# Performance work log

Hardware: AMD Instinct MI355X
Metric: run time of the kernel (lower is better)

The kernel has to match this reference:

```python
import jax, jax.numpy as jnp
import numpy as np

THETA = 10000.0

def _rope_cos_sin(seq_len, head_dim, dtype=jnp.float32):
    # matches precompute_freqs_cis: freqs over even indices of head_dim
    inv = 1.0 / (THETA ** (jnp.arange(0, head_dim, 2, dtype=jnp.float32) / head_dim))  # [hd/2]
    ang = jnp.arange(seq_len, dtype=jnp.float32)[:, None] * inv[None, :]               # [S, hd/2]
    return jnp.cos(ang).astype(dtype), jnp.sin(ang).astype(dtype)

def _apply_rope(x, cos, sin):
    # x: [b, h, s, d]; pairs are interleaved (d r) with r=2 -> complex (even=real, odd=imag)
    xe = x[..., 0::2]
    xo = x[..., 1::2]
    re = xe * cos - xo * sin
    im = xe * sin + xo * cos
    # interleave back: [..., d/2, 2] -> [..., d]
    return jnp.stack([re, im], axis=-1).reshape(x.shape)

def setup_inputs() -> dict:
    key = jax.random.key(0)
    ks = jax.random.split(key, 8)
    B, S, D = 2, 2048, 1024
    s = 0.02
    return {
        "query": jax.random.normal(ks[0], (B, S, D), jnp.float32),
        "key": jax.random.normal(ks[1], (B, S, D), jnp.float32),
        "value": jax.random.normal(ks[2], (B, S, D), jnp.float32),
        "q_w": jax.random.normal(ks[3], (D, D), jnp.float32) * s,
        "q_b": jnp.zeros((D,), jnp.float32),
        "k_w": jax.random.normal(ks[4], (D, D), jnp.float32) * s,
        "k_b": jnp.zeros((D,), jnp.float32),
        "v_w": jax.random.normal(ks[5], (D, D), jnp.float32) * s,
        "v_b": jnp.zeros((D,), jnp.float32),
        "o_w": jax.random.normal(ks[6], (D, D), jnp.float32) * s,
        "o_b": jnp.zeros((D,), jnp.float32),
    }

def reference(query, key, value, q_w, q_b, k_w, k_b, v_w, v_b, o_w, o_b):
    H = 16
    B, S, D = query.shape
    hd = D // H
    scaling = hd ** -0.5

    def split_heads(x):  # [b, s, (h d)] -> [b, h, s, d]
        return x.reshape(B, -1, H, hd).transpose(0, 2, 1, 3)

    q = split_heads(query @ q_w.T + q_b)
    k = split_heads(key @ k_w.T + k_b)
    v = split_heads(value @ v_w.T + v_b)

    cos, sin = _rope_cos_sin(S, hd)
    q = _apply_rope(q, cos, sin)
    k = _apply_rope(k, cos, sin)

    scores = jnp.einsum('bhqd,bhkd->bhqk', q, k) * scaling  # [B,H,S,S]
    attn = jax.nn.softmax(scores, axis=-1)
    out = jnp.einsum('bhqk,bhkd->bhqd', attn, v)            # [B,H,S,hd]
    out = out.transpose(0, 2, 1, 3).reshape(B, S, D)
    return out @ o_w.T + o_b
```

## Files before the change

### kernel.cpp

```cpp
#include <hip/hip_runtime.h>
#include <math.h>

#define B_  2
#define S_  2048
#define D_  1024
#define H_  16
#define HD_ 64
#define M_  (B_*S_)

typedef __attribute__((ext_vector_type(8))) short bf16x8;
typedef __attribute__((ext_vector_type(4))) float f32x4;
typedef unsigned short ushort_t;

#define MFMA32 __builtin_amdgcn_mfma_f32_16x16x32_bf16

__device__ inline unsigned short f2bf(float x) {
    unsigned u = __float_as_uint(x);
    unsigned r = (u + 0x7fff + ((u >> 16) & 1)) >> 16;
    return (unsigned short)r;
}
__device__ inline void gload16(const ushort_t* g, ushort_t* l) {
    __builtin_amdgcn_global_load_lds(
        (const __attribute__((address_space(1))) unsigned*)g,
        (__attribute__((address_space(3))) unsigned*)l, 16, 0, 0);
}

__global__ __launch_bounds__(256) void prep(
    const float* __restrict__ qa, const float* __restrict__ ka,
    const float* __restrict__ va,
    const float* __restrict__ qw, const float* __restrict__ kw,
    const float* __restrict__ vw, const float* __restrict__ ow,
    ushort_t* __restrict__ qab, ushort_t* __restrict__ kab,
    ushort_t* __restrict__ vab,
    ushort_t* __restrict__ qwb, ushort_t* __restrict__ kwb,
    ushort_t* __restrict__ vwb, ushort_t* __restrict__ owb,
    float* __restrict__ cost, float* __restrict__ sint)
{
    const int z = blockIdx.y;
    const int i = blockIdx.x * 256 + threadIdx.x;
    if (z == 7) {
        if (blockIdx.x >= (S_ * 32) / 256) return;
        int s = i >> 5, w = i & 31;
        double inv = pow(10000.0, -((double)(2 * w) / (double)HD_));
        double ang = (double)s * inv;
        cost[i] = (float)cos(ang);
        sint[i] = (float)sin(ang);
        return;
    }
    const float* in;
    ushort_t* dst;
    int n4;
    switch (z) {
        case 0: in = qa; dst = qab; n4 = (M_ * D_) / 4; break;
        case 1: in = ka; dst = kab; n4 = (M_ * D_) / 4; break;
        case 2: in = va; dst = vab; n4 = (M_ * D_) / 4; break;
        case 3: in = qw; dst = qwb; n4 = (D_ * D_) / 4; break;
        case 4: in = kw; dst = kwb; n4 = (D_ * D_) / 4; break;
        case 5: in = vw; dst = vwb; n4 = (D_ * D_) / 4; break;
        default: in = ow; dst = owb; n4 = (D_ * D_) / 4; break;
    }
    if (i >= n4) return;
    float4 v = ((const float4*)in)[i];
    unsigned short h0 = f2bf(v.x), h1 = f2bf(v.y), h2 = f2bf(v.z), h3 = f2bf(v.w);
    ((uint2*)dst)[i] = make_uint2((unsigned)h0 | ((unsigned)h1 << 16),
                                  (unsigned)h2 | ((unsigned)h3 << 16));
}

__global__ __launch_bounds__(256, 3) void fused_qkv(
    const ushort_t* __restrict__ A0, const ushort_t* __restrict__ A1,
    const ushort_t* __restrict__ A2,
    const ushort_t* __restrict__ W0, const ushort_t* __restrict__ W1,
    const ushort_t* __restrict__ W2,
    const float* __restrict__ b0, const float* __restrict__ b1,
    const float* __restrict__ b2,
    ushort_t* __restrict__ O0, ushort_t* __restrict__ O1,
    ushort_t* __restrict__ O2,
    const float* __restrict__ cost, const float* __restrict__ sint)
{
    __shared__ ushort_t Ab[12288];
    __shared__ ushort_t Wb[12288];

    const int tid  = threadIdx.x;
    const int wq   = tid >> 6;
    const int lane = tid & 63;
    const int l16  = lane & 15;
    const int quad = lane >> 4;

    const unsigned flat = blockIdx.x + (blockIdx.y << 3) + (blockIdx.z << 8);
    const unsigned xcd  = flat & 7;
    const unsigned slot = flat >> 3;
    const int z   = (int)(slot >> 5);
    const unsigned rr = slot & 31;
    const int bm  = (int)(xcd * 4 + (rr >> 3)) * 128;
    const int bn  = (int)(rr & 7) * 128;

    const ushort_t* A = z == 0 ? A0 : z == 1 ? A1 : A2;
    const ushort_t* W = z == 0 ? W0 : z == 1 ? W1 : W2;
    const float* bias = z == 0 ? b0 : z == 1 ? b1 : b2;

    const int m16 = tid & 15;
    const int akq = (tid >> 4) & 3;
    const int tw  = tid >> 6;

    const ushort_t* gA0 = A + (size_t)(bm + tw * 16 + m16) * D_ + akq * 8;
    const ushort_t* gA1 = gA0 + (size_t)64 * D_;
    const ushort_t* gW0 = W + (size_t)(bn + tw * 16 + m16) * D_ + akq * 8;
    const ushort_t* gW1 = gW0 + (size_t)64 * D_;

    const int wm = wq >> 1, wn = wq & 1;

    f32x4 acc[4][4];
#pragma unroll
    for (int mt = 0; mt < 4; ++mt)
#pragma unroll
        for (int nt = 0; nt < 4; ++nt)
            acc[mt][nt] = (f32x4){0.f, 0.f, 0.f, 0.f};

    gload16(gA0,      &Ab[tw * 512]);
    gload16(gA1,      &Ab[(tw + 4) * 512]);
    gload16(gW0,      &Wb[tw * 512]);
    gload16(gW1,      &Wb[(tw + 4) * 512]);
    gload16(gA0 + 32, &Ab[4096 + tw * 512]);
    gload16(gA1 + 32, &Ab[4096 + (tw + 4) * 512]);
    gload16(gW0 + 32, &Wb[4096 + tw * 512]);
    gload16(gW1 + 32, &Wb[4096 + (tw + 4) * 512]);

    int bcur = 0;
    for (int k = 0; k < 32; ++k) {
        if (k < 31) {
            asm volatile("s_waitcnt vmcnt(4)" ::: "memory");
        } else {
            asm volatile("s_waitcnt vmcnt(0)" ::: "memory");
        }
        __builtin_amdgcn_sched_barrier(0);
        __builtin_amdgcn_s_barrier();
        __builtin_amdgcn_sched_barrier(0);

        if (k < 30) {
            int bnx = bcur + 2; if (bnx >= 3) bnx -= 3;
            int ko = (k + 2) * 32;
            gload16(gA0 + ko, &Ab[bnx * 4096 + tw * 512]);
            gload16(gA1 + ko, &Ab[bnx * 4096 + (tw + 4) * 512]);
            gload16(gW0 + ko, &Wb[bnx * 4096 + tw * 512]);
            gload16(gW1 + ko, &Wb[bnx * 4096 + (tw + 4) * 512]);
        }

        const ushort_t* Abc = &Ab[bcur * 4096];
        const ushort_t* Wbc = &Wb[bcur * 4096];

        bf16x8 af[4], wf[4];
#pragma unroll
        for (int mt = 0; mt < 4; ++mt)
            af[mt] = *(const bf16x8*)&Abc[(wm * 4 + mt) * 512 + lane * 8];
#pragma unroll
        for (int nt = 0; nt < 4; ++nt)
            wf[nt] = *(const bf16x8*)&Wbc[(wn * 4 + nt) * 512 + lane * 8];
#pragma unroll
        for (int mt = 0; mt < 4; ++mt)
#pragma unroll
            for (int nt = 0; nt < 4; ++nt)
                acc[mt][nt] = MFMA32(af[mt], wf[nt], acc[mt][nt], 0, 0, 0);

        bcur += 1; if (bcur >= 3) bcur -= 3;
    }

    if (z == 0) {
        const float scale = 0.18033688011112042f;
#pragma unroll
        for (int mt = 0; mt < 4; ++mt) {
            int m = bm + wm * 64 + mt * 16 + quad * 4;
#pragma unroll
            for (int nt = 0; nt < 4; ++nt) {
                int n = bn + wn * 64 + nt * 16 + l16;
                float bb = bias[n];
                int h = n >> 6, d = n & 63, p = d >> 1;
#pragma unroll
                for (int r = 0; r < 4; ++r) {
                    int mm = m + r;
                    int s = mm & (S_ - 1), b = mm >> 11;
                    float x = acc[mt][nt][r] + bb;
                    float cs = cost[s * 32 + p], sn = sint[s * 32 + p];
                    float part = __shfl_xor(x, 1);
                    float y = (d & 1) ? (part * sn + x * cs)
                                      : (x * cs - part * sn);
                    O0[((size_t)(b * H_ + h) * S_ + s) * HD_ + d] = f2bf(y * scale);
                }
            }
        }
    } else if (z == 1) {
#pragma unroll
        for (int mt = 0; mt < 4; ++mt) {
            int m = bm + wm * 64 + mt * 16 + quad * 4;
#pragma unroll
            for (int nt = 0; nt < 4; ++nt) {
                int n = bn + wn * 64 + nt * 16 + l16;
                float bb = bias[n];
                int h = n >> 6, d = n & 63, p = d >> 1;
                int sub = ((d >> 5) & 1);
                int dq  = (d >> 3) & 3;
                int dj  = d & 7;
#pragma unroll
                for (int r = 0; r < 4; ++r) {
                    int mm = m + r;
                    int s = mm & (S_ - 1), b = mm >> 11;
                    float x = acc[mt][nt][r] + bb;
                    float cs = cost[s * 32 + p], sn = sint[s * 32 + p];
                    float part = __shfl_xor(x, 1);
                    float y = (d & 1) ? (part * sn + x * cs)
                                      : (x * cs - part * sn);
                    int kt  = s >> 5;
                    int st  = ((s >> 4) & 1) * 2 + sub;
                    size_t idx = ((size_t)(b * H_ + h) * 64 + kt) * 2048
                               + st * 512 + dq * 128 + (s & 15) * 8 + dj;
                    O1[idx] = f2bf(y);
                }
            }
        }
    } else {
#pragma unroll
        for (int mt = 0; mt < 4; ++mt) {
            int m = bm + wm * 64 + mt * 16 + quad * 4;
            int b = m >> 11, s0 = m & (S_ - 1);
            int vt = s0 >> 5;
            int kk = s0 & 31;
            int qd = (kk & 15) >> 2;
            int w0 = ((kk >> 4) & 1) * 4;
#pragma unroll
            for (int nt = 0; nt < 4; ++nt) {
                int n = bn + wn * 64 + nt * 16 + l16;
                float bb = bias[n];
                int h = n >> 6, d = n & 63;
                int mtv = d >> 4, dd = d & 15;
                unsigned short hh[4];
#pragma unroll
                for (int r = 0; r < 4; ++r)
                    hh[r] = f2bf(acc[mt][nt][r] + bb);
                size_t idx = ((size_t)(b * H_ + h) * 64 + vt) * 2048
                           + mtv * 512 + qd * 128 + dd * 8 + w0;
                *(uint2*)(O2 + idx) = make_uint2(
                    (unsigned)hh[0] | ((unsigned)hh[1] << 16),
                    (unsigned)hh[2] | ((unsigned)hh[3] << 16));
            }
        }
    }
}

__global__ __launch_bounds__(256, 2) void proj_o(
    const ushort_t* __restrict__ A, const ushort_t* __restrict__ W,
    const float* __restrict__ bias, float* __restrict__ outf)
{
    __shared__ ushort_t Ab[6144];
    __shared__ ushort_t Wb[12288];

    const int tid  = threadIdx.x;
    const int wq   = tid >> 6;
    const int lane = tid & 63;
    const int l16  = lane & 15;
    const int quad = lane >> 4;

    const unsigned flat = blockIdx.x + (blockIdx.y << 3);
    const unsigned xcd  = flat & 7;
    const unsigned slot = flat >> 3;
    const int bm = (int)(xcd * 8 + (slot >> 3)) * 64;
    const int bn = (int)(slot & 7) * 128;

    const int m16 = tid & 15;
    const int akq = (tid >> 4) & 3;
    const int tw  = tid >> 6;

    const ushort_t* gA  = A + (size_t)(bm + tw * 16 + m16) * D_ + akq * 8;
    const ushort_t* gW0 = W + (size_t)(bn + tw * 16 + m16) * D_ + akq * 8;
    const ushort_t* gW1 = gW0 + (size_t)64 * D_;

    const int wm = wq >> 1, wn = wq & 1;

    f32x4 acc[2][4];
#pragma unroll
    for (int mt = 0; mt < 2; ++mt)
#pragma unroll
        for (int nt = 0; nt < 4; ++nt)
            acc[mt][nt] = (f32x4){0.f, 0.f, 0.f, 0.f};

    gload16(gA,       &Ab[tw * 512]);
    gload16(gW0,      &Wb[tw * 512]);
    gload16(gW1,      &Wb[(tw + 4) * 512]);
    gload16(gA + 32,  &Ab[2048 + tw * 512]);
    gload16(gW0 + 32, &Wb[4096 + tw * 512]);
    gload16(gW1 + 32, &Wb[4096 + (tw + 4) * 512]);

    int bcur = 0;
    for (int k = 0; k < 32; ++k) {
        if (k < 31) {
            asm volatile("s_waitcnt vmcnt(3)" ::: "memory");
        } else {
            asm volatile("s_waitcnt vmcnt(0)" ::: "memory");
        }
        __builtin_amdgcn_sched_barrier(0);
        __builtin_amdgcn_s_barrier();
        __builtin_amdgcn_sched_barrier(0);

        if (k < 30) {
            int bnx = bcur + 2; if (bnx >= 3) bnx -= 3;
            int ko = (k + 2) * 32;
            gload16(gA  + ko, &Ab[bnx * 2048 + tw * 512]);
            gload16(gW0 + ko, &Wb[bnx * 4096 + tw * 512]);
            gload16(gW1 + ko, &Wb[bnx * 4096 + (tw + 4) * 512]);
        }

        const ushort_t* Abc = &Ab[bcur * 2048];
        const ushort_t* Wbc = &Wb[bcur * 4096];

        bf16x8 af[2], wf[4];
#pragma unroll
        for (int mt = 0; mt < 2; ++mt)
            af[mt] = *(const bf16x8*)&Abc[(wm * 2 + mt) * 512 + lane * 8];
#pragma unroll
        for (int nt = 0; nt < 4; ++nt)
            wf[nt] = *(const bf16x8*)&Wbc[(wn * 4 + nt) * 512 + lane * 8];
#pragma unroll
        for (int mt = 0; mt < 2; ++mt)
#pragma unroll
            for (int nt = 0; nt < 4; ++nt)
                acc[mt][nt] = MFMA32(af[mt], wf[nt], acc[mt][nt], 0, 0, 0);

        bcur += 1; if (bcur >= 3) bcur -= 3;
    }

#pragma unroll
    for (int mt = 0; mt < 2; ++mt) {
        int m = bm + wm * 32 + mt * 16 + quad * 4;
#pragma unroll
        for (int nt = 0; nt < 4; ++nt) {
            int n = bn + wn * 64 + nt * 16 + l16;
            float bb = bias[n];
#pragma unroll
            for (int r = 0; r < 4; ++r)
                outf[(size_t)(m + r) * D_ + n] = acc[mt][nt][r] + bb;
        }
    }
}

__global__ __launch_bounds__(256, 2) void attn_mfma(
    const ushort_t* __restrict__ Q, const ushort_t* __restrict__ Kf,
    const ushort_t* __restrict__ Vf, ushort_t* __restrict__ AO)
{
    __shared__ __align__(16) unsigned char SM[49152 + 512];
    float* MRG = (float*)SM;
    float* PSB = (float*)(SM + 49152);

    const int tid  = threadIdx.x;
    const int wq   = tid >> 6;
    const int lane = tid & 63;
    const int l16  = lane & 15;
    const int quad = lane >> 4;
    const int qg   = wq & 1;
    const int ks   = wq >> 1;

    const unsigned flat = blockIdx.x + (blockIdx.y << 4);
    const unsigned xcd  = flat & 7;
    const unsigned slot = flat >> 3;
    const int bh   = (int)(xcd * 4 + (slot >> 4));
    const int q0   = (int)(slot & 15) * 128 + qg * 64;

    bf16x8 qa[4][2];
#pragma unroll
    for (int nh = 0; nh < 4; ++nh)
#pragma unroll
        for (int c = 0; c < 2; ++c) {
            int row = q0 + nh * 16 + l16;
            qa[nh][c] = *(const bf16x8*)(Q + ((size_t)bh * S_ + row) * HD_
                                           + c * 32 + quad * 8);
        }
#pragma unroll
    for (int nh = 0; nh < 4; ++nh)
#pragma unroll
        for (int c = 0; c < 2; ++c)
            asm volatile("" : "+v"(qa[nh][c]));

    f32x4 oacc[4][4];
    f32x4 osum[4];
#pragma unroll
    for (int nh = 0; nh < 4; ++nh) {
        osum[nh] = (f32x4){0.f, 0.f, 0.f, 0.f};
#pragma unroll
        for (int mt = 0; mt < 4; ++mt)
            oacc[nh][mt] = (f32x4){0.f, 0.f, 0.f, 0.f};
    }

    const bf16x8 ones8 = {(short)0x3F80, (short)0x3F80, (short)0x3F80,
                          (short)0x3F80, (short)0x3F80, (short)0x3F80,
                          (short)0x3F80, (short)0x3F80};

    const ushort_t* Kbase = Kf + (size_t)bh * 64 * 2048;
    const ushort_t* Vbase = Vf + (size_t)bh * 64 * 2048;

#pragma unroll
    for (int t = 0; t < 2; ++t) {
        ushort_t* KB = (ushort_t*)(SM + t * 16384);
        ushort_t* VB = KB + 4096;
        const ushort_t* Kq = Kbase + (size_t)t * 4096;
        const ushort_t* Vq = Vbase + (size_t)t * 4096;
        gload16(Kq + tid * 8,        KB + tid * 8);
        gload16(Kq + 2048 + tid * 8, KB + 2048 + tid * 8);
        gload16(Vq + tid * 8,        VB + tid * 8);
        gload16(Vq + 2048 + tid * 8, VB + 2048 + tid * 8);
    }

    int cur = 0;
    for (int i = 0; i < 32; ++i) {
        if (i < 31) {
            asm volatile("s_waitcnt vmcnt(4)" ::: "memory");
        } else {
            asm volatile("s_waitcnt vmcnt(0)" ::: "memory");
        }
        __builtin_amdgcn_sched_barrier(0);
        __builtin_amdgcn_s_barrier();
        __builtin_amdgcn_sched_barrier(0);

        if (i < 30) {
            int nb = cur + 2; if (nb >= 3) nb -= 3;
            ushort_t* KB = (ushort_t*)(SM + nb * 16384);
            ushort_t* VB = KB + 4096;
            const ushort_t* Kq = Kbase + (size_t)(i + 2) * 4096;
            const ushort_t* Vq = Vbase + (size_t)(i + 2) * 4096;
            gload16(Kq + tid * 8,        KB + tid * 8);
            gload16(Kq + 2048 + tid * 8, KB + 2048 + tid * 8);
            gload16(Vq + tid * 8,        VB + tid * 8);
            gload16(Vq + 2048 + tid * 8, VB + 2048 + tid * 8);
        }

        const ushort_t* Kc = (const ushort_t*)(SM + cur * 16384) + ks * 2048;
        const ushort_t* Vc = (const ushort_t*)(SM + cur * 16384) + 4096 + ks * 2048;

        bf16x8 kf[2][2];
#pragma unroll
        for (int g = 0; g < 2; ++g)
#pragma unroll
            for (int c = 0; c < 2; ++c)
                kf[g][c] = *(const bf16x8*)&Kc[(g * 2 + c) * 512 + lane * 8];

        f32x4 s[4][2];
#pragma unroll
        for (int nh = 0; nh < 4; ++nh)
#pragma unroll
            for (int g = 0; g < 2; ++g)
                s[nh][g] = (f32x4){0.f, 0.f, 0.f, 0.f};
        __builtin_amdgcn_s_setprio(1);
#pragma unroll
        for (int c = 0; c < 2; ++c)
#pragma unroll
            for (int nh = 0; nh < 4; ++nh)
#pragma unroll
                for (int g = 0; g < 2; ++g)
                    s[nh][g] = MFMA32(kf[g][c], qa[nh][c], s[nh][g], 0, 0, 0);
        __builtin_amdgcn_s_setprio(0);

        bf16x8 pb8[4];
#pragma unroll
        for (int nh = 0; nh < 4; ++nh) {
            float p00 = __builtin_exp2f(s[nh][0][0]);
            float p01 = __builtin_exp2f(s[nh][0][1]);
            float p02 = __builtin_exp2f(s[nh][0][2]);
            float p03 = __builtin_exp2f(s[nh][0][3]);
            float p10 = __builtin_exp2f(s[nh][1][0]);
            float p11 = __builtin_exp2f(s[nh][1][1]);
            float p12 = __builtin_exp2f(s[nh][1][2]);
            float p13 = __builtin_exp2f(s[nh][1][3]);
            union { bf16x8 v; unsigned u[4]; } t;
            t.u[0] = __builtin_amdgcn_perm(__float_as_uint(p01),
                                           __float_as_uint(p00), 0x07060302);
            t.u[1] = __builtin_amdgcn_perm(__float_as_uint(p03),
                                           __float_as_uint(p02), 0x07060302);
            t.u[2] = __builtin_amdgcn_perm(__float_as_uint(p11),
                                           __float_as_uint(p10), 0x07060302);
            t.u[3] = __builtin_amdgcn_perm(__float_as_uint(p13),
                                           __float_as_uint(p12), 0x07060302);
            pb8[nh] = t.v;
        }

        __builtin_amdgcn_s_setprio(1);
#pragma unroll
        for (int mt = 0; mt < 4; ++mt) {
            bf16x8 vv = *(const bf16x8*)&Vc[mt * 512 + lane * 8];
#pragma unroll
            for (int nh = 0; nh < 4; ++nh)
                oacc[nh][mt] = MFMA32(vv, pb8[nh], oacc[nh][mt], 0, 0, 0);
        }
#pragma unroll
        for (int nh = 0; nh < 4; ++nh)
            osum[nh] = MFMA32(ones8, pb8[nh], osum[nh], 0, 0, 0);
        __builtin_amdgcn_s_setprio(0);

        cur += 1; if (cur >= 3) cur -= 3;
    }

    __syncthreads();

    if (ks == 1) {
#pragma unroll
        for (int nh = 0; nh < 4; ++nh) {
#pragma unroll
            for (int mt = 0; mt < 4; ++mt)
#pragma unroll
                for (int r = 0; r < 4; ++r)
                    MRG[(qg * 64 + nh * 16 + l16) * 65 + mt * 16 + quad * 4 + r]
                        = oacc[nh][mt][r];
            if (quad == 0)
                PSB[qg * 64 + nh * 16 + l16] = osum[nh][0];
        }
    }
    __syncthreads();
    if (ks == 0) {
        const int b = bh >> 4, h = bh & 15;
#pragma unroll
        for (int nh = 0; nh < 4; ++nh) {
            float pst = osum[nh][0] + PSB[qg * 64 + nh * 16 + l16];
            float inv = 1.0f / pst;
            int q = q0 + nh * 16 + l16;
#pragma unroll
            for (int mt = 0; mt < 4; ++mt) {
                unsigned short hh[4];
#pragma unroll
                for (int r = 0; r < 4; ++r) {
                    float x = oacc[nh][mt][r]
                        + MRG[(qg * 64 + nh * 16 + l16) * 65 + mt * 16 + quad * 4 + r];
                    hh[r] = f2bf(x * inv);
                }
                size_t base = ((size_t)b * S_ + q) * D_ + h * HD_
                            + mt * 16 + quad * 4;
                *(uint2*)(AO + base) = make_uint2(
                    (unsigned)hh[0] | ((unsigned)hh[1] << 16),
                    (unsigned)hh[2] | ((unsigned)hh[3] << 16));
            }
        }
    }
}

extern "C" void kernel_launch(void* const* d_in, const int* in_sizes, int n_in,
                              void* d_out, int out_size, void* d_ws, size_t ws_size,
                              hipStream_t stream) {
    const float* query = (const float*)d_in[0];
    const float* key   = (const float*)d_in[1];
    const float* value = (const float*)d_in[2];
    const float* q_w   = (const float*)d_in[3];
    const float* q_b   = (const float*)d_in[4];
    const float* k_w   = (const float*)d_in[5];
    const float* k_b   = (const float*)d_in[6];
    const float* v_w   = (const float*)d_in[7];
    const float* v_b   = (const float*)d_in[8];
    const float* o_w   = (const float*)d_in[9];
    const float* o_b   = (const float*)d_in[10];
    float* out = (float*)d_out;

    const size_t NT = (size_t)M_ * D_;
    const size_t WT = (size_t)D_ * D_;
    ushort_t* p = (ushort_t*)d_ws;
    ushort_t* qa_b = p; p += NT;
    ushort_t* ka_b = p; p += NT;
    ushort_t* va_b = p; p += NT;
    ushort_t* wqb  = p; p += WT;
    ushort_t* wkb  = p; p += WT;
    ushort_t* wvb  = p; p += WT;
    ushort_t* wob  = p; p += WT;
    ushort_t* Qb   = p; p += NT;
    ushort_t* Kfr  = p; p += NT;
    ushort_t* Vfr  = p; p += NT;
    ushort_t* AO   = p; p += NT;
    float* cost = (float*)p;
    float* sint = cost + (size_t)S_ * 32;

    dim3 gp((unsigned)(NT / 4 / 256), 8);
    prep<<<gp, 256, 0, stream>>>(query, key, value, q_w, k_w, v_w, o_w,
                                 qa_b, ka_b, va_b, wqb, wkb, wvb, wob,
                                 cost, sint);

    dim3 gq(D_ / 128, M_ / 128, 3);
    fused_qkv<<<gq, 256, 0, stream>>>(
        qa_b, ka_b, va_b, wqb, wkb, wvb,
        q_b, k_b, v_b, Qb, Kfr, Vfr, cost, sint);

    dim3 agrid(S_ / 128, B_ * H_);
    attn_mfma<<<agrid, 256, 0, stream>>>(Qb, Kfr, Vfr, AO);

    dim3 go(D_ / 128, M_ / 64);
    proj_o<<<go, 256, 0, stream>>>(AO, wob, o_b, out);
}
```

Before: 248.6 us.

## Restructure attention into 128-thread blocks without key-split merge

```diff
diff --git a/kernel.cpp b/kernel.cpp
--- a/kernel.cpp
+++ b/kernel.cpp
@@ -340,31 +340,27 @@
     }
 }
 
-__global__ __launch_bounds__(256, 2) void attn_mfma(
+__global__ __launch_bounds__(128, 3) void attn_mfma(
     const ushort_t* __restrict__ Q, const ushort_t* __restrict__ Kf,
     const ushort_t* __restrict__ Vf, ushort_t* __restrict__ AO)
 {
-    __shared__ __align__(16) unsigned char SM[49152 + 512];
-    float* MRG = (float*)SM;
-    float* PSB = (float*)(SM + 49152);
+    __shared__ __align__(16) ushort_t SMEM[3 * 4096];
 
     const int tid  = threadIdx.x;
     const int wq   = tid >> 6;
     const int lane = tid & 63;
     const int l16  = lane & 15;
     const int quad = lane >> 4;
-    const int qg   = wq & 1;
-    const int ks   = wq >> 1;
-
-    const unsigned flat = blockIdx.x + (blockIdx.y << 4);
+
+    const unsigned flat = blockIdx.x + (blockIdx.y << 5);
     const unsigned xcd  = flat & 7;
     const unsigned slot = flat >> 3;
-    const int bh   = (int)(xcd * 4 + (slot >> 4));
-    const int q0   = (int)(slot & 15) * 128 + qg * 64;
-
-    bf16x8 qa[4][2];
-#pragma unroll
-    for (int nh = 0; nh < 4; ++nh)
+    const int bh = (int)(xcd * 4 + (slot >> 5));
+    const int q0 = (int)(slot & 31) * 64 + wq * 32;
+
+    bf16x8 qa[2][2];
+#pragma unroll
+    for (int nh = 0; nh < 2; ++nh)
 #pragma unroll
         for (int c = 0; c < 2; ++c) {
             int row = q0 + nh * 16 + l16;
@@ -372,15 +368,15 @@
                                            + c * 32 + quad * 8);
         }
 #pragma unroll
-    for (int nh = 0; nh < 4; ++nh)
+    for (int nh = 0; nh < 2; ++nh)
 #pragma unroll
         for (int c = 0; c < 2; ++c)
             asm volatile("" : "+v"(qa[nh][c]));
 
-    f32x4 oacc[4][4];
-    f32x4 osum[4];
-#pragma unroll
-    for (int nh = 0; nh < 4; ++nh) {
+    f32x4 oacc[2][4];
+    f32x4 osum[2];
+#pragma unroll
+    for (int nh = 0; nh < 2; ++nh) {
         osum[nh] = (f32x4){0.f, 0.f, 0.f, 0.f};
 #pragma unroll
         for (int mt = 0; mt < 4; ++mt)
@@ -396,19 +392,18 @@
 
 #pragma unroll
     for (int t = 0; t < 2; ++t) {
-        ushort_t* KB = (ushort_t*)(SM + t * 16384);
-        ushort_t* VB = KB + 4096;
-        const ushort_t* Kq = Kbase + (size_t)t * 4096;
-        const ushort_t* Vq = Vbase + (size_t)t * 4096;
+        ushort_t* KB = &SMEM[t * 4096];
+        const ushort_t* Kq = Kbase + (size_t)t * 2048;
+        const ushort_t* Vq = Vbase + (size_t)t * 2048;
         gload16(Kq + tid * 8,        KB + tid * 8);
-        gload16(Kq + 2048 + tid * 8, KB + 2048 + tid * 8);
-        gload16(Vq + tid * 8,        VB + tid * 8);
-        gload16(Vq + 2048 + tid * 8, VB + 2048 + tid * 8);
+        gload16(Kq + 1024 + tid * 8, KB + 1024 + tid * 8);
+        gload16(Vq + tid * 8,        KB + 2048 + tid * 8);
+        gload16(Vq + 1024 + tid * 8, KB + 3072 + tid * 8);
     }
 
     int cur = 0;
-    for (int i = 0; i < 32; ++i) {
-        if (i < 31) {
+    for (int i = 0; i < 64; ++i) {
+        if (i < 63) {
             asm volatile("s_waitcnt vmcnt(4)" ::: "memory");
         } else {
             asm volatile("s_waitcnt vmcnt(0)" ::: "memory");
@@ -417,20 +412,19 @@
         __builtin_amdgcn_s_barrier();
         __builtin_amdgcn_sched_barrier(0);
 
-        if (i < 30) {
+        if (i < 62) {
             int nb = cur + 2; if (nb >= 3) nb -= 3;
-            ushort_t* KB = (ushort_t*)(SM + nb * 16384);
-            ushort_t* VB = KB + 4096;
-            const ushort_t* Kq = Kbase + (size_t)(i + 2) * 4096;
-            const ushort_t* Vq = Vbase + (size_t)(i + 2) * 4096;
+            ushort_t* KB = &SMEM[nb * 4096];
+            const ushort_t* Kq = Kbase + (size_t)(i + 2) * 2048;
+            const ushort_t* Vq = Vbase + (size_t)(i + 2) * 2048;
             gload16(Kq + tid * 8,        KB + tid * 8);
-            gload16(Kq + 2048 + tid * 8, KB + 2048 + tid * 8);
-            gload16(Vq + tid * 8,        VB + tid * 8);
-            gload16(Vq + 2048 + tid * 8, VB + 2048 + tid * 8);
-        }
-
-        const ushort_t* Kc = (const ushort_t*)(SM + cur * 16384) + ks * 2048;
-        const ushort_t* Vc = (const ushort_t*)(SM + cur * 16384) + 4096 + ks * 2048;
+            gload16(Kq + 1024 + tid * 8, KB + 1024 + tid * 8);
+            gload16(Vq + tid * 8,        KB + 2048 + tid * 8);
+            gload16(Vq + 1024 + tid * 8, KB + 3072 + tid * 8);
+        }
+
+        const ushort_t* Kc = &SMEM[cur * 4096];
+        const ushort_t* Vc = Kc + 2048;
 
         bf16x8 kf[2][2];
 #pragma unroll
@@ -439,9 +433,9 @@
             for (int c = 0; c < 2; ++c)
                 kf[g][c] = *(const bf16x8*)&Kc[(g * 2 + c) * 512 + lane * 8];
 
-        f32x4 s[4][2];
-#pragma unroll
-        for (int nh = 0; nh < 4; ++nh)
+        f32x4 s[2][2];
+#pragma unroll
+        for (int nh = 0; nh < 2; ++nh)
 #pragma unroll
             for (int g = 0; g < 2; ++g)
                 s[nh][g] = (f32x4){0.f, 0.f, 0.f, 0.f};
@@ -449,15 +443,15 @@
 #pragma unroll
         for (int c = 0; c < 2; ++c)
 #pragma unroll
-            for (int nh = 0; nh < 4; ++nh)
+            for (int nh = 0; nh < 2; ++nh)
 #pragma unroll
                 for (int g = 0; g < 2; ++g)
                     s[nh][g] = MFMA32(kf[g][c], qa[nh][c], s[nh][g], 0, 0, 0);
         __builtin_amdgcn_s_setprio(0);
 
-        bf16x8 pb8[4];
-#pragma unroll
-        for (int nh = 0; nh < 4; ++nh) {
+        bf16x8 pb8[2];
+#pragma unroll
+        for (int nh = 0; nh < 2; ++nh) {
             float p00 = __builtin_exp2f(s[nh][0][0]);
             float p01 = __builtin_exp2f(s[nh][0][1]);
             float p02 = __builtin_exp2f(s[nh][0][2]);
@@ -483,49 +477,29 @@
         for (int mt = 0; mt < 4; ++mt) {
             bf16x8 vv = *(const bf16x8*)&Vc[mt * 512 + lane * 8];
 #pragma unroll
-            for (int nh = 0; nh < 4; ++nh)
+            for (int nh = 0; nh < 2; ++nh)
                 oacc[nh][mt] = MFMA32(vv, pb8[nh], oacc[nh][mt], 0, 0, 0);
         }
 #pragma unroll
-        for (int nh = 0; nh < 4; ++nh)
+        for (int nh = 0; nh < 2; ++nh)
             osum[nh] = MFMA32(ones8, pb8[nh], osum[nh], 0, 0, 0);
         __builtin_amdgcn_s_setprio(0);
 
         cur += 1; if (cur >= 3) cur -= 3;
     }
 
-    __syncthreads();
-
-    if (ks == 1) {
-#pragma unroll
-        for (int nh = 0; nh < 4; ++nh) {
-#pragma unroll
-            for (int mt = 0; mt < 4; ++mt)
-#pragma unroll
-                for (int r = 0; r < 4; ++r)
-                    MRG[(qg * 64 + nh * 16 + l16) * 65 + mt * 16 + quad * 4 + r]
-                        = oacc[nh][mt][r];
-            if (quad == 0)
-                PSB[qg * 64 + nh * 16 + l16] = osum[nh][0];
-        }
-    }
-    __syncthreads();
-    if (ks == 0) {
+    {
         const int b = bh >> 4, h = bh & 15;
 #pragma unroll
-        for (int nh = 0; nh < 4; ++nh) {
-            float pst = osum[nh][0] + PSB[qg * 64 + nh * 16 + l16];
-            float inv = 1.0f / pst;
+        for (int nh = 0; nh < 2; ++nh) {
+            float inv = 1.0f / osum[nh][0];
             int q = q0 + nh * 16 + l16;
 #pragma unroll
             for (int mt = 0; mt < 4; ++mt) {
                 unsigned short hh[4];
 #pragma unroll
-                for (int r = 0; r < 4; ++r) {
-                    float x = oacc[nh][mt][r]
-                        + MRG[(qg * 64 + nh * 16 + l16) * 65 + mt * 16 + quad * 4 + r];
-                    hh[r] = f2bf(x * inv);
-                }
+                for (int r = 0; r < 4; ++r)
+                    hh[r] = f2bf(oacc[nh][mt][r] * inv);
                 size_t base = ((size_t)b * S_ + q) * D_ + h * HD_
                             + mt * 16 + quad * 4;
                 *(uint2*)(AO + base) = make_uint2(
@@ -579,8 +553,8 @@
         qa_b, ka_b, va_b, wqb, wkb, wvb,
         q_b, k_b, v_b, Qb, Kfr, Vfr, cost, sint);
 
-    dim3 agrid(S_ / 128, B_ * H_);
-    attn_mfma<<<agrid, 256, 0, stream>>>(Qb, Kfr, Vfr, AO);
+    dim3 agrid(S_ / 64, B_ * H_);
+    attn_mfma<<<agrid, 128, 0, stream>>>(Qb, Kfr, Vfr, AO);
 
     dim3 go(D_ / 128, M_ / 64);
     proj_o<<<go, 256, 0, stream>>>(AO, wob, o_b, out);
```

Measured after the change: 254.3 us. +2.3%, slower.

## Software-pipeline attention loop: overlap previous tile's PV MFMAs with exp2

Applied to the files above, without the earlier changes.

```diff
diff --git a/kernel.cpp b/kernel.cpp
--- a/kernel.cpp
+++ b/kernel.cpp
@@ -344,9 +344,9 @@
     const ushort_t* __restrict__ Q, const ushort_t* __restrict__ Kf,
     const ushort_t* __restrict__ Vf, ushort_t* __restrict__ AO)
 {
-    __shared__ __align__(16) unsigned char SM[49152 + 512];
+    __shared__ __align__(16) unsigned char SM[65536 + 512];
     float* MRG = (float*)SM;
-    float* PSB = (float*)(SM + 49152);
+    float* PSB = (float*)(SM + 65536);
 
     const int tid  = threadIdx.x;
     const int wq   = tid >> 6;
@@ -391,22 +391,25 @@
                           (short)0x3F80, (short)0x3F80, (short)0x3F80,
                           (short)0x3F80, (short)0x3F80};
 
+    bf16x8 pb8p[4];
+#pragma unroll
+    for (int nh = 0; nh < 4; ++nh)
+        pb8p[nh] = (bf16x8){0, 0, 0, 0, 0, 0, 0, 0};
+
     const ushort_t* Kbase = Kf + (size_t)bh * 64 * 2048;
     const ushort_t* Vbase = Vf + (size_t)bh * 64 * 2048;
 
 #pragma unroll
     for (int t = 0; t < 2; ++t) {
         ushort_t* KB = (ushort_t*)(SM + t * 16384);
-        ushort_t* VB = KB + 4096;
         const ushort_t* Kq = Kbase + (size_t)t * 4096;
         const ushort_t* Vq = Vbase + (size_t)t * 4096;
         gload16(Kq + tid * 8,        KB + tid * 8);
         gload16(Kq + 2048 + tid * 8, KB + 2048 + tid * 8);
-        gload16(Vq + tid * 8,        VB + tid * 8);
-        gload16(Vq + 2048 + tid * 8, VB + 2048 + tid * 8);
-    }
-
-    int cur = 0;
+        gload16(Vq + tid * 8,        KB + 4096 + tid * 8);
+        gload16(Vq + 2048 + tid * 8, KB + 4096 + 2048 + tid * 8);
+    }
+
     for (int i = 0; i < 32; ++i) {
         if (i < 31) {
             asm volatile("s_waitcnt vmcnt(4)" ::: "memory");
@@ -418,19 +421,19 @@
         __builtin_amdgcn_sched_barrier(0);
 
         if (i < 30) {
-            int nb = cur + 2; if (nb >= 3) nb -= 3;
+            const int nb = (i + 2) & 3;
             ushort_t* KB = (ushort_t*)(SM + nb * 16384);
-            ushort_t* VB = KB + 4096;
             const ushort_t* Kq = Kbase + (size_t)(i + 2) * 4096;
             const ushort_t* Vq = Vbase + (size_t)(i + 2) * 4096;
             gload16(Kq + tid * 8,        KB + tid * 8);
             gload16(Kq + 2048 + tid * 8, KB + 2048 + tid * 8);
-            gload16(Vq + tid * 8,        VB + tid * 8);
-            gload16(Vq + 2048 + tid * 8, VB + 2048 + tid * 8);
-        }
-
-        const ushort_t* Kc = (const ushort_t*)(SM + cur * 16384) + ks * 2048;
-        const ushort_t* Vc = (const ushort_t*)(SM + cur * 16384) + 4096 + ks * 2048;
+            gload16(Vq + tid * 8,        KB + 4096 + tid * 8);
+            gload16(Vq + 2048 + tid * 8, KB + 4096 + 2048 + tid * 8);
+        }
+
+        const ushort_t* Kc = (const ushort_t*)(SM + (i & 3) * 16384) + ks * 2048;
+        const int vb = i ? ((i - 1) & 3) : 0;
+        const ushort_t* Vc = (const ushort_t*)(SM + vb * 16384) + 4096 + ks * 2048;
 
         bf16x8 kf[2][2];
 #pragma unroll
@@ -438,6 +441,10 @@
 #pragma unroll
             for (int c = 0; c < 2; ++c)
                 kf[g][c] = *(const bf16x8*)&Kc[(g * 2 + c) * 512 + lane * 8];
+        bf16x8 vv[4];
+#pragma unroll
+        for (int mt = 0; mt < 4; ++mt)
+            vv[mt] = *(const bf16x8*)&Vc[mt * 512 + lane * 8];
 
         f32x4 s[4][2];
 #pragma unroll
@@ -453,9 +460,17 @@
 #pragma unroll
                 for (int g = 0; g < 2; ++g)
                     s[nh][g] = MFMA32(kf[g][c], qa[nh][c], s[nh][g], 0, 0, 0);
+
+#pragma unroll
+        for (int mt = 0; mt < 4; ++mt)
+#pragma unroll
+            for (int nh = 0; nh < 4; ++nh)
+                oacc[nh][mt] = MFMA32(vv[mt], pb8p[nh], oacc[nh][mt], 0, 0, 0);
+#pragma unroll
+        for (int nh = 0; nh < 4; ++nh)
+            osum[nh] = MFMA32(ones8, pb8p[nh], osum[nh], 0, 0, 0);
         __builtin_amdgcn_s_setprio(0);
 
-        bf16x8 pb8[4];
 #pragma unroll
         for (int nh = 0; nh < 4; ++nh) {
             float p00 = __builtin_exp2f(s[nh][0][0]);
@@ -475,23 +490,22 @@
                                            __float_as_uint(p10), 0x07060302);
             t.u[3] = __builtin_amdgcn_perm(__float_as_uint(p13),
                                            __float_as_uint(p12), 0x07060302);
-            pb8[nh] = t.v;
-        }
-
-        __builtin_amdgcn_s_setprio(1);
+            pb8p[nh] = t.v;
+        }
+    }
+
+    {
+        const ushort_t* Vc = (const ushort_t*)(SM + 3 * 16384) + 4096 + ks * 2048;
 #pragma unroll
         for (int mt = 0; mt < 4; ++mt) {
             bf16x8 vv = *(const bf16x8*)&Vc[mt * 512 + lane * 8];
 #pragma unroll
             for (int nh = 0; nh < 4; ++nh)
-                oacc[nh][mt] = MFMA32(vv, pb8[nh], oacc[nh][mt], 0, 0, 0);
+                oacc[nh][mt] = MFMA32(vv, pb8p[nh], oacc[nh][mt], 0, 0, 0);
         }
 #pragma unroll
         for (int nh = 0; nh < 4; ++nh)
-            osum[nh] = MFMA32(ones8, pb8[nh], osum[nh], 0, 0, 0);
-        __builtin_amdgcn_s_setprio(0);
-
-        cur += 1; if (cur >= 3) cur -= 3;
+            osum[nh] = MFMA32(ones8, pb8p[nh], osum[nh], 0, 0, 0);
     }
 
     __syncthreads();
```

New measurement: 248.3 us. No clear change (-0.1%).

## Load attention K/V fragments directly into registers with double-buffered prefetch

Applied to the files above, without the earlier changes.

```diff
diff --git a/kernel.cpp b/kernel.cpp
--- a/kernel.cpp
+++ b/kernel.cpp
@@ -340,13 +340,76 @@
     }
 }
 
+__device__ __forceinline__ void attn_body(
+    bf16x8 (&KR)[4], bf16x8 (&VR)[4], int i,
+    const bf16x8 (&qa)[4][2], f32x4 (&oacc)[4][4], f32x4 (&osum)[4],
+    const bf16x8& ones8, const ushort_t* kp, const ushort_t* vp)
+{
+    f32x4 s[4][2];
+#pragma unroll
+    for (int nh = 0; nh < 4; ++nh)
+#pragma unroll
+        for (int g = 0; g < 2; ++g)
+            s[nh][g] = (f32x4){0.f, 0.f, 0.f, 0.f};
+    __builtin_amdgcn_s_setprio(1);
+#pragma unroll
+    for (int c = 0; c < 2; ++c)
+#pragma unroll
+        for (int nh = 0; nh < 4; ++nh)
+#pragma unroll
+            for (int g = 0; g < 2; ++g)
+                s[nh][g] = MFMA32(KR[g * 2 + c], qa[nh][c], s[nh][g], 0, 0, 0);
+    __builtin_amdgcn_s_setprio(0);
+
+    bf16x8 pb8[4];
+#pragma unroll
+    for (int nh = 0; nh < 4; ++nh) {
+        float p00 = __builtin_exp2f(s[nh][0][0]);
+        float p01 = __builtin_exp2f(s[nh][0][1]);
+        float p02 = __builtin_exp2f(s[nh][0][2]);
+        float p03 = __builtin_exp2f(s[nh][0][3]);
+        float p10 = __builtin_exp2f(s[nh][1][0]);
+        float p11 = __builtin_exp2f(s[nh][1][1]);
+        float p12 = __builtin_exp2f(s[nh][1][2]);
+        float p13 = __builtin_exp2f(s[nh][1][3]);
+        union { bf16x8 v; unsigned u[4]; } t;
+        t.u[0] = __builtin_amdgcn_perm(__float_as_uint(p01),
+                                       __float_as_uint(p00), 0x07060302);
+        t.u[1] = __builtin_amdgcn_perm(__float_as_uint(p03),
+                                       __float_as_uint(p02), 0x07060302);
+        t.u[2] = __builtin_amdgcn_perm(__float_as_uint(p11),
+                                       __float_as_uint(p10), 0x07060302);
+        t.u[3] = __builtin_amdgcn_perm(__float_as_uint(p13),
+                                       __float_as_uint(p12), 0x07060302);
+        pb8[nh] = t.v;
+    }
+
+    __builtin_amdgcn_s_setprio(1);
+#pragma unroll
+    for (int mt = 0; mt < 4; ++mt)
+#pragma unroll
+        for (int nh = 0; nh < 4; ++nh)
+            oacc[nh][mt] = MFMA32(VR[mt], pb8[nh], oacc[nh][mt], 0, 0, 0);
+#pragma unroll
+    for (int nh = 0; nh < 4; ++nh)
+        osum[nh] = MFMA32(ones8, pb8[nh], osum[nh], 0, 0, 0);
+    __builtin_amdgcn_s_setprio(0);
+
+    if (i + 2 < 32) {
+#pragma unroll
+        for (int j = 0; j < 4; ++j) {
+            KR[j] = *(const bf16x8*)(kp + (size_t)(i + 2) * 4096 + j * 512);
+            VR[j] = *(const bf16x8*)(vp + (size_t)(i + 2) * 4096 + j * 512);
+        }
+    }
+}
+
 __global__ __launch_bounds__(256, 2) void attn_mfma(
     const ushort_t* __restrict__ Q, const ushort_t* __restrict__ Kf,
     const ushort_t* __restrict__ Vf, ushort_t* __restrict__ AO)
 {
-    __shared__ __align__(16) unsigned char SM[49152 + 512];
-    float* MRG = (float*)SM;
-    float* PSB = (float*)(SM + 49152);
+    __shared__ float MRG[128 * 65];
+    __shared__ float PSB[128];
 
     const int tid  = threadIdx.x;
     const int wq   = tid >> 6;
@@ -391,110 +454,22 @@
                           (short)0x3F80, (short)0x3F80, (short)0x3F80,
                           (short)0x3F80, (short)0x3F80};
 
-    const ushort_t* Kbase = Kf + (size_t)bh * 64 * 2048;
-    const ushort_t* Vbase = Vf + (size_t)bh * 64 * 2048;
-
-#pragma unroll
-    for (int t = 0; t < 2; ++t) {
-        ushort_t* KB = (ushort_t*)(SM + t * 16384);
-        ushort_t* VB = KB + 4096;
-        const ushort_t* Kq = Kbase + (size_t)t * 4096;
-        const ushort_t* Vq = Vbase + (size_t)t * 4096;
-        gload16(Kq + tid * 8,        KB + tid * 8);
-        gload16(Kq + 2048 + tid * 8, KB + 2048 + tid * 8);
-        gload16(Vq + tid * 8,        VB + tid * 8);
-        gload16(Vq + 2048 + tid * 8, VB + 2048 + tid * 8);
-    }
-
-    int cur = 0;
-    for (int i = 0; i < 32; ++i) {
-        if (i < 31) {
-            asm volatile("s_waitcnt vmcnt(4)" ::: "memory");
-        } else {
-            asm volatile("s_waitcnt vmcnt(0)" ::: "memory");
-        }
-        __builtin_amdgcn_sched_barrier(0);
-        __builtin_amdgcn_s_barrier();
-        __builtin_amdgcn_sched_barrier(0);
-
-        if (i < 30) {
-            int nb = cur + 2; if (nb >= 3) nb -= 3;
-            ushort_t* KB = (ushort_t*)(SM + nb * 16384);
-            ushort_t* VB = KB + 4096;
-            const ushort_t* Kq = Kbase + (size_t)(i + 2) * 4096;
-            const ushort_t* Vq = Vbase + (size_t)(i + 2) * 4096;
-            gload16(Kq + tid * 8,        KB + tid * 8);
-            gload16(Kq + 2048 + tid * 8, KB + 2048 + tid * 8);
-            gload16(Vq + tid * 8,        VB + tid * 8);
-            gload16(Vq + 2048 + tid * 8, VB + 2048 + tid * 8);
-        }
-
-        const ushort_t* Kc = (const ushort_t*)(SM + cur * 16384) + ks * 2048;
-        const ushort_t* Vc = (const ushort_t*)(SM + cur * 16384) + 4096 + ks * 2048;
-
-        bf16x8 kf[2][2];
-#pragma unroll
-        for (int g = 0; g < 2; ++g)
-#pragma unroll
-            for (int c = 0; c < 2; ++c)
-                kf[g][c] = *(const bf16x8*)&Kc[(g * 2 + c) * 512 + lane * 8];
-
-        f32x4 s[4][2];
-#pragma unroll
-        for (int nh = 0; nh < 4; ++nh)
-#pragma unroll
-            for (int g = 0; g < 2; ++g)
-                s[nh][g] = (f32x4){0.f, 0.f, 0.f, 0.f};
-        __builtin_amdgcn_s_setprio(1);
-#pragma unroll
-        for (int c = 0; c < 2; ++c)
-#pragma unroll
-            for (int nh = 0; nh < 4; ++nh)
-#pragma unroll
-                for (int g = 0; g < 2; ++g)
-                    s[nh][g] = MFMA32(kf[g][c], qa[nh][c], s[nh][g], 0, 0, 0);
-        __builtin_amdgcn_s_setprio(0);
-
-        bf16x8 pb8[4];
-#pragma unroll
-        for (int nh = 0; nh < 4; ++nh) {
-            float p00 = __builtin_exp2f(s[nh][0][0]);
-            float p01 = __builtin_exp2f(s[nh][0][1]);
-            float p02 = __builtin_exp2f(s[nh][0][2]);
-            float p03 = __builtin_exp2f(s[nh][0][3]);
-            float p10 = __builtin_exp2f(s[nh][1][0]);
-            float p11 = __builtin_exp2f(s[nh][1][1]);
-            float p12 = __builtin_exp2f(s[nh][1][2]);
-            float p13 = __builtin_exp2f(s[nh][1][3]);
-            union { bf16x8 v; unsigned u[4]; } t;
-            t.u[0] = __builtin_amdgcn_perm(__float_as_uint(p01),
-                                           __float_as_uint(p00), 0x07060302);
-            t.u[1] = __builtin_amdgcn_perm(__float_as_uint(p03),
-                                           __float_as_uint(p02), 0x07060302);
-            t.u[2] = __builtin_amdgcn_perm(__float_as_uint(p11),
-                                           __float_as_uint(p10), 0x07060302);
-            t.u[3] = __builtin_amdgcn_perm(__float_as_uint(p13),
-                                           __float_as_uint(p12), 0x07060302);
-            pb8[nh] = t.v;
-        }
-
-        __builtin_amdgcn_s_setprio(1);
-#pragma unroll
-        for (int mt = 0; mt < 4; ++mt) {
-            bf16x8 vv = *(const bf16x8*)&Vc[mt * 512 + lane * 8];
-#pragma unroll
-            for (int nh = 0; nh < 4; ++nh)
-                oacc[nh][mt] = MFMA32(vv, pb8[nh], oacc[nh][mt], 0, 0, 0);
-        }
-#pragma unroll
-        for (int nh = 0; nh < 4; ++nh)
-            osum[nh] = MFMA32(ones8, pb8[nh], osum[nh], 0, 0, 0);
-        __builtin_amdgcn_s_setprio(0);
-
-        cur += 1; if (cur >= 3) cur -= 3;
-    }
-
-    __syncthreads();
+    const ushort_t* kp = Kf + (size_t)bh * 131072 + ks * 2048 + lane * 8;
+    const ushort_t* vp = Vf + (size_t)bh * 131072 + ks * 2048 + lane * 8;
+
+    bf16x8 kA[4], vA[4], kB[4], vB[4];
+#pragma unroll
+    for (int j = 0; j < 4; ++j) {
+        kA[j] = *(const bf16x8*)(kp + j * 512);
+        vA[j] = *(const bf16x8*)(vp + j * 512);
+        kB[j] = *(const bf16x8*)(kp + 4096 + j * 512);
+        vB[j] = *(const bf16x8*)(vp + 4096 + j * 512);
+    }
+
+    for (int i = 0; i < 32; i += 2) {
+        attn_body(kA, vA, i,     qa, oacc, osum, ones8, kp, vp);
+        attn_body(kB, vB, i + 1, qa, oacc, osum, ones8, kp, vp);
+    }
 
     if (ks == 1) {
 #pragma unroll
```

New measurement: 246.4 us. No clear change (-0.9%).
